# Kernel optimization log

Hardware: AMD Instinct MI355X
Metric: run time of the kernel (lower is better)

## Reference

```python
import jax, jax.numpy as jnp
import numpy as np

HIDDEN = 4096
N_HEADS = 32
N_KV_HEADS = 8
HEAD_DIM = HIDDEN // N_HEADS          # 128
GROUP = N_HEADS // N_KV_HEADS         # 4 q-heads per kv-head
Q_SIZE = N_HEADS * HEAD_DIM           # 4096
KV_SIZE = N_KV_HEADS * HEAD_DIM       # 1024
T = 2048


def setup_inputs() -> dict:
    key = jax.random.key(0)
    k1, k2, k3 = jax.random.split(key, 3)
    positions = jnp.arange(T, dtype=jnp.int64) if jax.config.jax_enable_x64 else jnp.arange(T, dtype=jnp.int32)
    hidden_states = jax.random.normal(k1, (T, HIDDEN), dtype=jnp.float32)
    # torch.nn.Linear weights: out = x @ W.T
    w_qkv = jax.random.normal(k2, (Q_SIZE + 2 * KV_SIZE, HIDDEN), dtype=jnp.float32) * 0.02
    w_o = jax.random.normal(k3, (HIDDEN, HIDDEN), dtype=jnp.float32) * 0.02
    return {"positions": positions, "hidden_states": hidden_states, "w_qkv": w_qkv, "w_o": w_o}


def reference(positions, hidden_states, w_qkv, w_o):
    del positions  # rotary is a no-op in the fake module
    t = hidden_states.shape[0]
    scaling = HEAD_DIM ** -0.5

    qkv = hidden_states @ w_qkv.T                              # [T, q+2kv]
    q, k, v = jnp.split(qkv, [Q_SIZE, Q_SIZE + KV_SIZE], axis=-1)
    # GQA mapping: q-head h uses kv-head h // GROUP (contiguous groups)
    q = q.reshape(t, N_KV_HEADS, GROUP, HEAD_DIM)              # [T, Hkv, G, d]
    k = k.reshape(t, N_KV_HEADS, HEAD_DIM)                     # [T, Hkv, d]
    v = v.reshape(t, N_KV_HEADS, HEAD_DIM)

    # Cache starts empty -> token i attends to keys 0..i (causal prefill)
    logits = jnp.einsum('tkgd,skd->kgts', q, k) * scaling      # [Hkv, G, T, T]
    causal = jnp.tril(jnp.ones((t, t), dtype=bool))            # s <= t
    logits = jnp.where(causal, logits, jnp.finfo(logits.dtype).min)
    weights = jax.nn.softmax(logits, axis=-1)
    ctx = jnp.einsum('kgts,skd->tkgd', weights, v)             # [T, Hkv, G, d]
    ctx = ctx.reshape(t, HIDDEN)
    return ctx @ w_o.T
```

## Files before the change

### kernel.cpp

```cpp
#include <hip/hip_runtime.h>

typedef unsigned short u16;
typedef __bf16 bf16x8 __attribute__((ext_vector_type(8)));
typedef float f32x4 __attribute__((ext_vector_type(4)));

__device__ __forceinline__ u16 f2bf(float f) {
  union { float f; unsigned u; } v; v.f = f;
  unsigned r = v.u + 0x7FFFu + ((v.u >> 16) & 1u);
  return (u16)(r >> 16);
}

__device__ __forceinline__ void gload16(const void* g, void* l) {
  __builtin_amdgcn_global_load_lds(
      (const __attribute__((address_space(1))) unsigned int*)g,
      (__attribute__((address_space(3))) unsigned int*)l, 16, 0, 0);
}

__global__ __launch_bounds__(256) void cvt_bf16(const float* __restrict__ in,
                                                u16* __restrict__ out, long n) {
  long i = ((long)blockIdx.x * 256 + threadIdx.x) * 8;
  const long stride = (long)gridDim.x * 2048;
  for (; i < n; i += stride) {
    float4 a = *(const float4*)(in + i);
    float4 b = *(const float4*)(in + i + 4);
    uint4 o;
    o.x = (unsigned)f2bf(a.x) | ((unsigned)f2bf(a.y) << 16);
    o.y = (unsigned)f2bf(a.z) | ((unsigned)f2bf(a.w) << 16);
    o.z = (unsigned)f2bf(b.x) | ((unsigned)f2bf(b.y) << 16);
    o.w = (unsigned)f2bf(b.z) | ((unsigned)f2bf(b.w) << 16);
    *(uint4*)(out + i) = o;
  }
}

template <int BM, int BN, typename OUT>
__global__ __launch_bounds__(512, 2) void gemmQ(const u16* __restrict__ A,
                                                const u16* __restrict__ B,
                                                OUT* __restrict__ C,
                                                int M, int N, int K) {
  constexpr int MREP = BM / 32;
  constexpr int NREP = BN / 64;
  constexpr int MQ = MREP / 4;
  constexpr int QS = MQ * 16;
  constexpr int AI = BM / 64;
  constexpr int BI = BN / 64;
  constexpr int TE = AI + BI;
  static_assert(MREP % 4 == 0, "need 4 m-quarters");
  __shared__ __align__(16) u16 sA[2][BM * 64];
  __shared__ __align__(16) u16 sB[2][BN * 64];

  const int tid = threadIdx.x;
  const int w = tid >> 6, ln = tid & 63;
  const int lr = ln & 15, lg = ln >> 4;
  const int wr = w >> 2, wc = w & 3;

  const int nN = N / BN;
  const int bm = ((int)blockIdx.x / nN) * BM;
  const int bn = ((int)blockIdx.x % nN) * BN;

  const int s_r = tid >> 3;
  const int scol = (((tid & 7) * 16) ^ ((s_r & 7) << 4)) >> 1;
  const int gA0 = ((s_r / QS) & 1) * (BM / 2) + (s_r / (2 * QS)) * QS +
                  (s_r & (QS - 1));
  const u16* pAb = A + (size_t)(bm + gA0) * K + scol;
  const u16* pBb = B + (size_t)(bn + s_r) * K + scol;

  const int mask = (lr & 7) << 4;
  const int pBr = (wc * (BN / 4) + lr) * 128;

  f32x4 acc[MREP][NREP] = {};
  const int nk = K >> 6;

  auto stage1 = [&](int buf, int k0, int j) {
    if (j < BI)
      gload16(pBb + (size_t)j * 64 * K + k0, (char*)sB[buf] + j * 8192 + tid * 16);
    else {
      const int i = j - BI;
      gload16(pAb + (size_t)i * 32 * K + k0, (char*)sA[buf] + i * 8192 + tid * 16);
    }
  };

#pragma unroll
  for (int j = 0; j < TE; ++j) stage1(0, 0, j);

  constexpr int S[4] = {0, 2, 4, TE - AI / 2};
  constexpr int E[4] = {2, 4, TE - AI / 2, TE};

#pragma unroll 1
  for (int t = 0; t < nk; ++t) {
    const int buf = t & 1;
    const int k1 = (t + 1) << 6;
    const bool more = (t + 1 < nk);
    const char* lA = (const char*)sA[buf];
    const char* lB = (const char*)sB[buf];

    bf16x8 bfr[NREP][2];
#pragma unroll
    for (int q = 0; q < 4; ++q) {
      if (q == 0) {
        if constexpr (AI == 4) asm volatile("s_waitcnt vmcnt(2)" ::: "memory");
        else                   asm volatile("s_waitcnt vmcnt(1)" ::: "memory");
      } else if (q == 2) {
        if (more) asm volatile("s_waitcnt vmcnt(4)" ::: "memory");
        else      asm volatile("s_waitcnt vmcnt(0)" ::: "memory");
      }
      __builtin_amdgcn_s_barrier();
      __builtin_amdgcn_sched_barrier(0);

      if (q == 0) {
#pragma unroll
        for (int nf = 0; nf < NREP; ++nf)
#pragma unroll
          for (int s = 0; s < 2; ++s)
            bfr[nf][s] = *(const bf16x8*)(lB + pBr + nf * 2048 +
                                          ((lg * 16 + s * 64) ^ mask));
      }
      bf16x8 af[MQ][2];
#pragma unroll
      for (int j = 0; j < MQ; ++j)
#pragma unroll
        for (int s = 0; s < 2; ++s)
          af[j][s] = *(const bf16x8*)(
              lA + (q * 2 * QS + wr * QS + j * 16 + lr) * 128 +
              ((lg * 16 + s * 64) ^ mask));

      if (more) {
#pragma unroll
        for (int j = S[q]; j < E[q]; ++j) stage1(buf ^ 1, k1, j);
      }

      asm volatile("s_waitcnt lgkmcnt(0)" ::: "memory");
      __builtin_amdgcn_sched_barrier(0);
      __builtin_amdgcn_s_setprio(1);
#pragma unroll
      for (int s = 0; s < 2; ++s)
#pragma unroll
        for (int j = 0; j < MQ; ++j)
#pragma unroll
          for (int nf = 0; nf < NREP; ++nf)
            acc[q * MQ + j][nf] = __builtin_amdgcn_mfma_f32_16x16x32_bf16(
                af[j][s], bfr[nf][s], acc[q * MQ + j][nf], 0, 0, 0);
      __builtin_amdgcn_s_setprio(0);
    }
  }

#pragma unroll
  for (int m = 0; m < MREP; ++m)
#pragma unroll
    for (int nf = 0; nf < NREP; ++nf)
#pragma unroll
      for (int r = 0; r < 4; ++r) {
        const int row = bm + wr * (BM / 2) + m * 16 + lg * 4 + r;
        const int col = bn + wc * (BN / 4) + nf * 16 + lr;
        const float v = acc[m][nf][r];
        if constexpr (sizeof(OUT) == 2)
          C[(size_t)row * N + col] = (OUT)f2bf(v);
        else
          C[(size_t)row * N + col] = v;
      }
}

__global__ __launch_bounds__(256) void vtrans(const u16* __restrict__ qkv,
                                              u16* __restrict__ vT) {
  __shared__ u16 tile[128][65];
  const int hk = blockIdx.y;
  const int tb = blockIdx.x * 64;
  const int tid = threadIdx.x;
#pragma unroll
  for (int p = 0; p < 4; ++p) {
    const int tr = p * 16 + (tid >> 4);
    const int d0 = (tid & 15) * 8;
    const uint4 x = *(const uint4*)(qkv + (size_t)(tb + tr) * 6144 + 5120 + hk * 128 + d0);
    const u16* xv = (const u16*)&x;
#pragma unroll
    for (int j = 0; j < 8; ++j) tile[d0 + j][tr] = xv[j];
  }
  __syncthreads();
#pragma unroll
  for (int p = 0; p < 4; ++p) {
    const int d = p * 32 + (tid >> 3);
    const int t0 = (tid & 7) * 8;
    u16 v[8];
#pragma unroll
    for (int j = 0; j < 8; ++j) v[j] = tile[d][t0 + j];
    uint4 o;
    unsigned* ov = (unsigned*)&o;
#pragma unroll
    for (int j = 0; j < 4; ++j)
      ov[j] = (unsigned)v[2 * j] | ((unsigned)v[2 * j + 1] << 16);
    *(uint4*)(vT + (size_t)hk * 128 * 2048 + (size_t)d * 2048 + tb + t0) = o;
  }
}

__global__ __launch_bounds__(256) void attn(const u16* __restrict__ qkv,
                                            const u16* __restrict__ vT,
                                            u16* __restrict__ ctx) {
  __shared__ __align__(16) u16 sK[2][64 * 128];
  __shared__ __align__(16) u16 sV[2][128 * 64];
  __shared__ __align__(16) u16 sP[4 * 16 * 64];
  const int tid = threadIdx.x, w = tid >> 6, ln = tid & 63;
  const int lr = ln & 15, lg = ln >> 4;
  const int h = blockIdx.y, hk = h >> 2;
  const int pi = blockIdx.x;

  const float scale = 0.08838834764831845f;
  const float LOG2E = 1.4426950408889634f;
  char* const pw = (char*)sP + w * 2048;

  auto stage = [&](int buf, int kt) {
    const int kvbase = kt * 64;
#pragma unroll
    for (int i = 0; i < 4; ++i) {
      const int off = i * 4096 + tid * 16;
      {
        const int row = off >> 8, cbp = off & 255;
        const int cb = cbp ^ ((row & 7) << 4);
        gload16(qkv + (size_t)(kvbase + row) * 6144 + 4096 + hk * 128 + (cb >> 1),
                (char*)sK + buf * 16384 + off);
      }
      {
        const int row = off >> 7, cbp = off & 127;
        const int cb = cbp ^ ((row & 7) << 4);
        gload16(vT + (size_t)hk * 262144 + (size_t)row * 2048 + kvbase + (cb >> 1),
                (char*)sV + buf * 16384 + off);
      }
    }
  };

#pragma unroll 1
  for (int ph = 0; ph < 2; ++ph) {
    const int qt = ph ? (31 - pi) : pi;
    const int qbase = qt * 64;
    const int nkt = qt + 1;

    bf16x8 qf[4];
    {
      const u16* qrow = qkv + (size_t)(qbase + w * 16 + lr) * 6144 + h * 128 + lg * 8;
#pragma unroll
      for (int kk = 0; kk < 4; ++kk) qf[kk] = *(const bf16x8*)(qrow + kk * 32);
    }

    f32x4 acc_o[8] = {};
    float m_r[4] = {-INFINITY, -INFINITY, -INFINITY, -INFINITY};
    float l_r[4] = {0.f, 0.f, 0.f, 0.f};

    stage(0, 0);

#pragma unroll 1
    for (int kt = 0; kt < nkt; ++kt) {
      const int buf = kt & 1;
      const int kvbase = kt * 64;
      __syncthreads();
      if (kt + 1 < nkt) stage(buf ^ 1, kt + 1);

      char* const kbase = (char*)sK + buf * 16384;
      char* const vbase = (char*)sV + buf * 16384;

      f32x4 sacc[4] = {};
#pragma unroll
      for (int kk = 0; kk < 4; ++kk) {
#pragma unroll
        for (int nf = 0; nf < 4; ++nf) {
          const int row = nf * 16 + lr;
          const int byt = row * 256 + ((kk * 64 + lg * 16) ^ ((row & 7) << 4));
          const bf16x8 kf = *(const bf16x8*)(kbase + byt);
          sacc[nf] = __builtin_amdgcn_mfma_f32_16x16x32_bf16(qf[kk], kf, sacc[nf], 0, 0, 0);
        }
      }

      const bool diag = (kt == qt);
      float p[4][4];
#pragma unroll
      for (int r = 0; r < 4; ++r) {
        const int qrow = qbase + w * 16 + lg * 4 + r;
        float mx = -INFINITY;
#pragma unroll
        for (int nf = 0; nf < 4; ++nf) {
          float v = sacc[nf][r] * scale;
          if (diag && (kvbase + nf * 16 + lr > qrow)) v = -INFINITY;
          p[nf][r] = v;
          mx = fmaxf(mx, v);
        }
        mx = fmaxf(mx, __shfl_xor(mx, 1));
        mx = fmaxf(mx, __shfl_xor(mx, 2));
        mx = fmaxf(mx, __shfl_xor(mx, 4));
        mx = fmaxf(mx, __shfl_xor(mx, 8));
        const float mt = fmaxf(m_r[r], mx);
        const float alpha = exp2f((m_r[r] - mt) * LOG2E);
        m_r[r] = mt;
        float rs = 0.f;
#pragma unroll
        for (int nf = 0; nf < 4; ++nf) {
          const float e = exp2f((p[nf][r] - mt) * LOG2E);
          p[nf][r] = e;
          rs += e;
        }
        rs += __shfl_xor(rs, 1);
        rs += __shfl_xor(rs, 2);
        rs += __shfl_xor(rs, 4);
        rs += __shfl_xor(rs, 8);
        l_r[r] = l_r[r] * alpha + rs;
#pragma unroll
        for (int o = 0; o < 8; ++o) acc_o[o][r] = acc_o[o][r] * alpha;
      }

#pragma unroll
      for (int r = 0; r < 4; ++r) {
        const int row = lg * 4 + r;
#pragma unroll
        for (int nf = 0; nf < 4; ++nf) {
          const int col = nf * 16 + lr;
          const int byt = row * 128 + ((2 * col) ^ ((row & 7) << 4));
          *(u16*)(pw + byt) = f2bf(p[nf][r]);
        }
      }

#pragma unroll
      for (int kk2 = 0; kk2 < 2; ++kk2) {
        const int pbyt = lr * 128 + ((kk2 * 64 + lg * 16) ^ ((lr & 7) << 4));
        const bf16x8 pf = *(const bf16x8*)(pw + pbyt);
#pragma unroll
        for (int o = 0; o < 8; ++o) {
          const int vrow = o * 16 + lr;
          const int vbyt = vrow * 128 + ((kk2 * 64 + lg * 16) ^ ((vrow & 7) << 4));
          const bf16x8 vf = *(const bf16x8*)(vbase + vbyt);
          acc_o[o] = __builtin_amdgcn_mfma_f32_16x16x32_bf16(pf, vf, acc_o[o], 0, 0, 0);
        }
      }
    }

#pragma unroll
    for (int r = 0; r < 4; ++r) {
      const float inv = 1.f / l_r[r];
      const int t = qbase + w * 16 + lg * 4 + r;
#pragma unroll
      for (int o = 0; o < 8; ++o)
        ctx[(size_t)t * 4096 + h * 128 + o * 16 + lr] = f2bf(acc_o[o][r] * inv);
    }
    __syncthreads();
  }
}

extern "C" void kernel_launch(void* const* d_in, const int* in_sizes, int n_in,
                              void* d_out, int out_size, void* d_ws, size_t ws_size,
                              hipStream_t stream) {
  (void)in_sizes; (void)n_in; (void)out_size; (void)ws_size;
  const float* hidden = (const float*)d_in[1];
  const float* w_qkv = (const float*)d_in[2];
  const float* w_o = (const float*)d_in[3];
  float* out = (float*)d_out;
  char* ws = (char*)d_ws;

  u16* xb    = (u16*)(ws + 0);
  u16* wqkvb = (u16*)(ws + 16777216);
  u16* wob   = (u16*)(ws + 67108864);
  u16* qkvb  = (u16*)(ws + 100663296);
  u16* vTb   = (u16*)(ws + 125829120);
  u16* ctxb  = (u16*)(ws + 130023424);

  cvt_bf16<<<4096, 256, 0, stream>>>(hidden, xb, (long)2048 * 4096);
  cvt_bf16<<<8192, 256, 0, stream>>>(w_qkv, wqkvb, (long)6144 * 4096);
  cvt_bf16<<<8192, 256, 0, stream>>>(w_o, wob, (long)4096 * 4096);
  gemmQ<256, 192, u16><<<256, 512, 0, stream>>>(xb, wqkvb, qkvb, 2048, 6144, 4096);
  vtrans<<<dim3(32, 8), 256, 0, stream>>>(qkvb, vTb);
  attn<<<dim3(16, 32), 256, 0, stream>>>(qkvb, vTb, ctxb);
  gemmQ<128, 256, float><<<256, 512, 0, stream>>>(ctxb, wob, out, 2048, 4096, 4096);
}
```

Measured before the change: 334.6 us.

## Restructure GEMM main loop with split-k LDS reads and counted lgkm waits

The GEMM k-loop is rewritten so B fragments for both k-halves are read once per tile, and the first quarter's MFMAs start after only the first half of the LDS reads complete, using a counted lgkmcnt wait. A-fragment reads for the next quarter are issued before the barrier, ping-ponging between two register sets so LDS latency overlaps MFMA work. Global-to-LDS prefetch issue is redistributed across quarters with adjusted vmcnt thresholds. This costs more registers, and hand-counted wait values must match the issue order exactly for both tile shapes.

```diff
diff --git a/kernel.cpp b/kernel.cpp
--- a/kernel.cpp
+++ b/kernel.cpp
@@ -33,7 +33,7 @@
 }
 
 template <int BM, int BN, typename OUT>
-__global__ __launch_bounds__(512, 2) void gemmQ(const u16* __restrict__ A,
+__global__ __launch_bounds__(512, 2) void gemmR(const u16* __restrict__ A,
                                                 const u16* __restrict__ B,
                                                 OUT* __restrict__ C,
                                                 int M, int N, int K) {
@@ -43,8 +43,7 @@
   constexpr int QS = MQ * 16;
   constexpr int AI = BM / 64;
   constexpr int BI = BN / 64;
-  constexpr int TE = AI + BI;
-  static_assert(MREP % 4 == 0, "need 4 m-quarters");
+  static_assert(NREP + MQ == 5, "counted lgkm assumes 5");
   __shared__ __align__(16) u16 sA[2][BM * 64];
   __shared__ __align__(16) u16 sB[2][BN * 64];
 
@@ -70,77 +69,142 @@
   f32x4 acc[MREP][NREP] = {};
   const int nk = K >> 6;
 
-  auto stage1 = [&](int buf, int k0, int j) {
-    if (j < BI)
-      gload16(pBb + (size_t)j * 64 * K + k0, (char*)sB[buf] + j * 8192 + tid * 16);
-    else {
-      const int i = j - BI;
-      gload16(pAb + (size_t)i * 32 * K + k0, (char*)sA[buf] + i * 8192 + tid * 16);
-    }
+  auto stB = [&](int buf, int k0, int j) {
+    gload16(pBb + (size_t)j * 64 * K + k0, (char*)sB[buf] + j * 8192 + tid * 16);
   };
-
-#pragma unroll
-  for (int j = 0; j < TE; ++j) stage1(0, 0, j);
-
-  constexpr int S[4] = {0, 2, 4, TE - AI / 2};
-  constexpr int E[4] = {2, 4, TE - AI / 2, TE};
+  auto stA = [&](int buf, int k0, int i) {
+    gload16(pAb + (size_t)i * 32 * K + k0, (char*)sA[buf] + i * 8192 + tid * 16);
+  };
+  auto rdB = [&](const char* lB, int s, bf16x8* dst) {
+#pragma unroll
+    for (int nf = 0; nf < NREP; ++nf)
+      dst[nf] = *(const bf16x8*)(lB + pBr + nf * 2048 +
+                                 ((lg * 16 + s * 64) ^ mask));
+  };
+  auto rdA = [&](const char* lA, int q, int s, bf16x8* dst) {
+#pragma unroll
+    for (int j = 0; j < MQ; ++j)
+      dst[j] = *(const bf16x8*)(lA + (q * 2 * QS + wr * QS + j * 16 + lr) * 128 +
+                                ((lg * 16 + s * 64) ^ mask));
+  };
+
+#pragma unroll
+  for (int j = 0; j < BI; ++j) stB(0, 0, j);
+#pragma unroll
+  for (int i = 0; i < AI; ++i) stA(0, 0, i);
 
 #pragma unroll 1
   for (int t = 0; t < nk; ++t) {
     const int buf = t & 1;
+    const char* lA = (const char*)sA[buf];
+    const char* lB = (const char*)sB[buf];
     const int k1 = (t + 1) << 6;
     const bool more = (t + 1 < nk);
-    const char* lA = (const char*)sA[buf];
-    const char* lB = (const char*)sB[buf];
-
-    bf16x8 bfr[NREP][2];
-#pragma unroll
-    for (int q = 0; q < 4; ++q) {
-      if (q == 0) {
-        if constexpr (AI == 4) asm volatile("s_waitcnt vmcnt(2)" ::: "memory");
-        else                   asm volatile("s_waitcnt vmcnt(1)" ::: "memory");
-      } else if (q == 2) {
-        if (more) asm volatile("s_waitcnt vmcnt(4)" ::: "memory");
-        else      asm volatile("s_waitcnt vmcnt(0)" ::: "memory");
-      }
-      __builtin_amdgcn_s_barrier();
+
+    if constexpr (AI == 4) asm volatile("s_waitcnt vmcnt(2)" ::: "memory");
+    else                   asm volatile("s_waitcnt vmcnt(1)" ::: "memory");
+    __builtin_amdgcn_sched_barrier(0);
+    __builtin_amdgcn_s_barrier();
+    __builtin_amdgcn_sched_barrier(0);
+
+    bf16x8 bfr[2][NREP];
+    bf16x8 afA[2][MQ], afB[2][MQ];
+
+    rdB(lB, 0, bfr[0]); rdA(lA, 0, 0, afA[0]);
+    rdB(lB, 1, bfr[1]); rdA(lA, 0, 1, afA[1]);
+    asm volatile("s_waitcnt lgkmcnt(5)" ::: "memory");
+    __builtin_amdgcn_sched_barrier(0);
+    __builtin_amdgcn_s_setprio(1);
+#pragma unroll
+    for (int j = 0; j < MQ; ++j)
+#pragma unroll
+      for (int nf = 0; nf < NREP; ++nf)
+        acc[j][nf] = __builtin_amdgcn_mfma_f32_16x16x32_bf16(
+            afA[0][j], bfr[0][nf], acc[j][nf], 0, 0, 0);
+    __builtin_amdgcn_s_setprio(0);
+    asm volatile("s_waitcnt lgkmcnt(0)" ::: "memory");
+    __builtin_amdgcn_sched_barrier(0);
+    __builtin_amdgcn_s_setprio(1);
+#pragma unroll
+    for (int j = 0; j < MQ; ++j)
+#pragma unroll
+      for (int nf = 0; nf < NREP; ++nf)
+        acc[j][nf] = __builtin_amdgcn_mfma_f32_16x16x32_bf16(
+            afA[1][j], bfr[1][nf], acc[j][nf], 0, 0, 0);
+    __builtin_amdgcn_s_setprio(0);
+    rdA(lA, 1, 0, afB[0]); rdA(lA, 1, 1, afB[1]);
+    if (more) {
+      stB(buf ^ 1, k1, 0); stB(buf ^ 1, k1, 1);
+      if constexpr (BI >= 3) stB(buf ^ 1, k1, 2);
+    }
+    __builtin_amdgcn_sched_barrier(0);
+    __builtin_amdgcn_s_barrier();
+
+    asm volatile("s_waitcnt lgkmcnt(0)" ::: "memory");
+    __builtin_amdgcn_sched_barrier(0);
+    __builtin_amdgcn_s_setprio(1);
+#pragma unroll
+    for (int s = 0; s < 2; ++s)
+#pragma unroll
+      for (int j = 0; j < MQ; ++j)
+#pragma unroll
+        for (int nf = 0; nf < NREP; ++nf)
+          acc[MQ + j][nf] = __builtin_amdgcn_mfma_f32_16x16x32_bf16(
+              afB[s][j], bfr[s][nf], acc[MQ + j][nf], 0, 0, 0);
+    __builtin_amdgcn_s_setprio(0);
+    if constexpr (AI == 4) {
+      if (more) asm volatile("s_waitcnt vmcnt(4)" ::: "memory");
+      else      asm volatile("s_waitcnt vmcnt(1)" ::: "memory");
+    } else {
+      if (more) asm volatile("s_waitcnt vmcnt(2)" ::: "memory");
+      else      asm volatile("s_waitcnt vmcnt(0)" ::: "memory");
+    }
+    __builtin_amdgcn_sched_barrier(0);
+    rdA(lA, 2, 0, afA[0]); rdA(lA, 2, 1, afA[1]);
+    if (more) {
+      if constexpr (BI == 3) { stA(buf ^ 1, k1, 0); stA(buf ^ 1, k1, 1); }
+      else { stB(buf ^ 1, k1, 2); stB(buf ^ 1, k1, 3);
+             stA(buf ^ 1, k1, 0); stA(buf ^ 1, k1, 1); }
+    }
+    __builtin_amdgcn_sched_barrier(0);
+    __builtin_amdgcn_s_barrier();
+
+    asm volatile("s_waitcnt lgkmcnt(0)" ::: "memory");
+    __builtin_amdgcn_sched_barrier(0);
+    __builtin_amdgcn_s_setprio(1);
+#pragma unroll
+    for (int s = 0; s < 2; ++s)
+#pragma unroll
+      for (int j = 0; j < MQ; ++j)
+#pragma unroll
+        for (int nf = 0; nf < NREP; ++nf)
+          acc[2 * MQ + j][nf] = __builtin_amdgcn_mfma_f32_16x16x32_bf16(
+              afA[s][j], bfr[s][nf], acc[2 * MQ + j][nf], 0, 0, 0);
+    __builtin_amdgcn_s_setprio(0);
+    if constexpr (AI == 4) {
+      if (more) asm volatile("s_waitcnt vmcnt(5)" ::: "memory");
+      else      asm volatile("s_waitcnt vmcnt(0)" ::: "memory");
       __builtin_amdgcn_sched_barrier(0);
-
-      if (q == 0) {
+    }
+    rdA(lA, 3, 0, afB[0]); rdA(lA, 3, 1, afB[1]);
+    if (more) {
+      if constexpr (BI == 3) { stA(buf ^ 1, k1, 2); stA(buf ^ 1, k1, 3); }
+    }
+    __builtin_amdgcn_sched_barrier(0);
+    __builtin_amdgcn_s_barrier();
+
+    asm volatile("s_waitcnt lgkmcnt(0)" ::: "memory");
+    __builtin_amdgcn_sched_barrier(0);
+    __builtin_amdgcn_s_setprio(1);
+#pragma unroll
+    for (int s = 0; s < 2; ++s)
+#pragma unroll
+      for (int j = 0; j < MQ; ++j)
 #pragma unroll
         for (int nf = 0; nf < NREP; ++nf)
-#pragma unroll
-          for (int s = 0; s < 2; ++s)
-            bfr[nf][s] = *(const bf16x8*)(lB + pBr + nf * 2048 +
-                                          ((lg * 16 + s * 64) ^ mask));
-      }
-      bf16x8 af[MQ][2];
-#pragma unroll
-      for (int j = 0; j < MQ; ++j)
-#pragma unroll
-        for (int s = 0; s < 2; ++s)
-          af[j][s] = *(const bf16x8*)(
-              lA + (q * 2 * QS + wr * QS + j * 16 + lr) * 128 +
-              ((lg * 16 + s * 64) ^ mask));
-
-      if (more) {
-#pragma unroll
-        for (int j = S[q]; j < E[q]; ++j) stage1(buf ^ 1, k1, j);
-      }
-
-      asm volatile("s_waitcnt lgkmcnt(0)" ::: "memory");
-      __builtin_amdgcn_sched_barrier(0);
-      __builtin_amdgcn_s_setprio(1);
-#pragma unroll
-      for (int s = 0; s < 2; ++s)
-#pragma unroll
-        for (int j = 0; j < MQ; ++j)
-#pragma unroll
-          for (int nf = 0; nf < NREP; ++nf)
-            acc[q * MQ + j][nf] = __builtin_amdgcn_mfma_f32_16x16x32_bf16(
-                af[j][s], bfr[nf][s], acc[q * MQ + j][nf], 0, 0, 0);
-      __builtin_amdgcn_s_setprio(0);
-    }
+          acc[3 * MQ + j][nf] = __builtin_amdgcn_mfma_f32_16x16x32_bf16(
+              afB[s][j], bfr[s][nf], acc[3 * MQ + j][nf], 0, 0, 0);
+    __builtin_amdgcn_s_setprio(0);
   }
 
 #pragma unroll
@@ -360,8 +424,8 @@
   cvt_bf16<<<4096, 256, 0, stream>>>(hidden, xb, (long)2048 * 4096);
   cvt_bf16<<<8192, 256, 0, stream>>>(w_qkv, wqkvb, (long)6144 * 4096);
   cvt_bf16<<<8192, 256, 0, stream>>>(w_o, wob, (long)4096 * 4096);
-  gemmQ<256, 192, u16><<<256, 512, 0, stream>>>(xb, wqkvb, qkvb, 2048, 6144, 4096);
+  gemmR<256, 192, u16><<<256, 512, 0, stream>>>(xb, wqkvb, qkvb, 2048, 6144, 4096);
   vtrans<<<dim3(32, 8), 256, 0, stream>>>(qkvb, vTb);
   attn<<<dim3(16, 32), 256, 0, stream>>>(qkvb, vTb, ctxb);
-  gemmQ<128, 256, float><<<256, 512, 0, stream>>>(ctxb, wob, out, 2048, 4096, 4096);
-}
+  gemmR<128, 256, float><<<256, 512, 0, stream>>>(ctxb, wob, out, 2048, 4096, 4096);
+}
```

Result: no change. 336.5 us (+0.6%).
